# Performance work log

Measured on AMD Instinct MI355X. Metric: run time of the kernel, lower is better.

The kernel has to match this reference:

```python
import jax, jax.numpy as jnp
import numpy as np
from jax import lax

# Key identity used: modulating ALL weights of output channel o by s_o (with no bias
# inside the modulated conv, as in the source where F.conv2d(..., bias=None)) is
# mathematically identical to a plain conv followed by per-(batch, out_channel)
# scaling of the output. This collapses the per-sample Python loop into one conv.

def _upsample2x(x):
    # nearest-neighbor x2, matching F.interpolate(scale_factor=2) default mode
    return jnp.repeat(jnp.repeat(x, 2, axis=2), 2, axis=3)

def _conv(x, w):
    return lax.conv_general_dilated(
        x, w, window_strides=(1, 1), padding=[(1, 1), (1, 1)],
        dimension_numbers=("NCHW", "OIHW", "NCHW"))

def _modconv(x, style, w, fc_w, fc_b):
    # style_fc: [B, style_dim] -> [B, out_ch]
    s = style @ fc_w.T + fc_b          # [B, O]
    y = _conv(x, w)                    # [B, O, H, W]
    return y * s[:, :, None, None]


def setup_inputs() -> dict:
    key = jax.random.key(0)
    ks = jax.random.split(key, 16)
    B, SD = 8, 512
    chans = [(512, 256), (256, 128), (128, 64), (64, 64), (64, 64)]
    inp = {
        "x": jax.random.normal(ks[0], (B, 512, 8, 8), jnp.float32),
        "style": jax.random.normal(ks[1], (B, SD), jnp.float32),
    }
    for i, (ci, co) in enumerate(chans, start=1):
        inp[f"w{i}"] = jax.random.normal(ks[2 * i], (co, ci, 3, 3), jnp.float32) * (1.0 / np.sqrt(ci * 9))
        inp[f"fw{i}"] = jax.random.normal(ks[2 * i + 1], (co, SD), jnp.float32) * (1.0 / np.sqrt(SD))
        inp[f"fb{i}"] = jnp.ones((co,), jnp.float32)
    inp["wf"] = jax.random.normal(ks[12], (3, 64, 3, 3), jnp.float32) * (1.0 / np.sqrt(64 * 9))
    inp["bf"] = jnp.zeros((3,), jnp.float32)
    return inp


def reference(x, style, w1, fw1, fb1, w2, fw2, fb2, w3, fw3, fb3,
              w4, fw4, fb4, w5, fw5, fb5, wf, bf):
    x = _upsample2x(x)
    x = jax.nn.relu(_modconv(x, style, w1, fw1, fb1))
    x = _upsample2x(x)
    x = jax.nn.relu(_modconv(x, style, w2, fw2, fb2))
    x = _upsample2x(x)
    x = jax.nn.relu(_modconv(x, style, w3, fw3, fb3))
    x = _upsample2x(x)
    x = jax.nn.relu(_modconv(x, style, w4, fw4, fb4))
    x = _upsample2x(x)
    x = jax.nn.relu(_modconv(x, style, w5, fw5, fb5))
    x = _conv(x, wf) + bf[None, :, None, None]
    return x
```

## Files before the change

kernel.cpp:

```cpp
#include <hip/hip_runtime.h>
#include <hip/hip_bf16.h>
#include <cstddef>

typedef __bf16 bf16x8 __attribute__((ext_vector_type(8)));
typedef float f32x4 __attribute__((ext_vector_type(4)));

__global__ void prep_all_kernel(const float* __restrict__ x, __hip_bfloat16* __restrict__ act0,
                                const float* __restrict__ w1, __hip_bfloat16* __restrict__ o1,
                                const float* __restrict__ w2, __hip_bfloat16* __restrict__ o2,
                                const float* __restrict__ w3, __hip_bfloat16* __restrict__ o3,
                                const float* __restrict__ w4, __hip_bfloat16* __restrict__ o4,
                                const float* __restrict__ w5, __hip_bfloat16* __restrict__ o5,
                                const float* __restrict__ wf, __hip_bfloat16* __restrict__ of,
                                const float* __restrict__ style,
                                const float* __restrict__ fw1, const float* __restrict__ fb1,
                                const float* __restrict__ fw2, const float* __restrict__ fb2,
                                const float* __restrict__ fw3, const float* __restrict__ fb3,
                                const float* __restrict__ fw4, const float* __restrict__ fb4,
                                const float* __restrict__ fw5, const float* __restrict__ fb5,
                                float* __restrict__ S) {
    const int blk = blockIdx.x;
    if (blk < 1024) {
        int t = blk * 256 + threadIdx.x;
        int c = t & 511; int rest = t >> 9;
        int w = rest & 7; rest >>= 3; int h = rest & 7; int b = rest >> 3;
        act0[t] = __float2bfloat16(x[((b * 512 + c) * 8 + h) * 8 + w]);
    } else if (blk < 12324) {
        int t = (blk - 1024) * 256 + threadIdx.x;
        if (t < 2752512) {
            const float* w; __hip_bfloat16* o; int CI, lgCICH, lgCO16;
            if      (t < 2097152) { w = w1; o = o1; CI = 512; lgCICH = 3; lgCO16 = 4; }
            else if (t < 2621440) { t -= 2097152; w = w2; o = o2; CI = 256; lgCICH = 2; lgCO16 = 3; }
            else                  { t -= 2621440; w = w3; o = o3; CI = 128; lgCICH = 1; lgCO16 = 2; }
            int j    = t & 7;
            int ln   = (t >> 3) & 63;
            int ch   = (t >> 9) & 1;
            int cich = (t >> 10) & ((1 << lgCICH) - 1);
            int co16 = (t >> (10 + lgCICH)) & ((1 << lgCO16) - 1);
            int tap  = (t >> (10 + lgCICH + lgCO16)) & 3;
            int cls  = (t >> (12 + lgCICH + lgCO16)) & 3;
            int co = co16 * 16 + (ln & 15);
            int ci = cich * 64 + ch * 32 + (ln >> 4) * 8 + j;
            int py = cls >> 1, px = cls & 1;
            int i = tap >> 1, jj = tap & 1;
            int r0 = i * (1 + py), rc = py ? (2 - i) : (1 + i);
            int c0 = jj * (1 + px), cc = px ? (2 - jj) : (1 + jj);
            const float* wb = w + ((size_t)co * CI + ci) * 9;
            float s = 0.f;
            for (int rr = 0; rr < rc; ++rr)
                for (int c2 = 0; c2 < cc; ++c2)
                    s += wb[(r0 + rr) * 3 + (c0 + c2)];
            o[t] = __float2bfloat16(s);
        } else if (t < 2883584) {
            int u = t - 2752512;
            const float* w; __hip_bfloat16* o;
            if (u < 65536) { w = w4; o = o4; }
            else           { u -= 65536; w = w5; o = o5; }
            int j   = u & 7;
            int ln  = (u >> 3) & 63;
            int ch  = (u >> 9) & 1;
            int nt  = (u >> 10) & 3;
            int tp  = (u >> 12) & 3;
            int cls = (u >> 14) & 3;
            int py = cls >> 1, px = cls & 1;
            int i = tp >> 1, jj = tp & 1;
            int co = nt * 16 + (ln & 15);
            int ci = ch * 32 + (ln >> 4) * 8 + j;
            int r0 = i * (1 + py), rc = py ? (2 - i) : (1 + i);
            int c0 = jj * (1 + px), cc = px ? (2 - jj) : (1 + jj);
            const float* wb = w + ((size_t)co * 64 + ci) * 9;
            float s = 0.f;
            for (int rr = 0; rr < rc; ++rr)
                for (int c2 = 0; c2 < cc; ++c2)
                    s += wb[(r0 + rr) * 3 + (c0 + c2)];
            o[u] = __float2bfloat16(s);
        } else if (t < 2892800) {
            int u = t - 2883584;
            int j  = u & 7;
            int ln = (u >> 3) & 63;
            int ch = (u >> 9) & 1;
            int tap = u >> 10;
            int rr = ln & 15, qq = ln >> 4;
            int ci = ch * 32 + qq * 8 + j;
            float v = (rr < 3) ? wf[((size_t)rr * 64 + ci) * 9 + tap] : 0.f;
            of[u] = __float2bfloat16(v);
        }
    } else {
        int wvid = (blk - 12324) * 4 + (threadIdx.x >> 6);
        int lane = threadIdx.x & 63;
        const float* fw; const float* fb; int lg, sOff, local;
        if      (wvid < 2048) { fw = fw1; fb = fb1; lg = 8; sOff = 0;    local = wvid; }
        else if (wvid < 3072) { fw = fw2; fb = fb2; lg = 7; sOff = 2048; local = wvid - 2048; }
        else if (wvid < 3584) { fw = fw3; fb = fb3; lg = 6; sOff = 3072; local = wvid - 3072; }
        else if (wvid < 4096) { fw = fw4; fb = fb4; lg = 6; sOff = 3584; local = wvid - 3584; }
        else                  { fw = fw5; fb = fb5; lg = 6; sOff = 4096; local = wvid - 4096; }
        int b = local >> lg, o = local & ((1 << lg) - 1);
        const float* sb = style + b * 512;
        const float* fwo = fw + (size_t)o * 512;
        float p = 0.f;
        #pragma unroll
        for (int k = lane; k < 512; k += 64) p += sb[k] * fwo[k];
        #pragma unroll
        for (int off = 32; off > 0; off >>= 1) p += __shfl_down(p, off);
        if (lane == 0) S[sOff + local] = p + fb[o];
    }
}

template <int CI, int CO, int HS, int WS>
__launch_bounds__(512)
__global__ void conv_partial_kernel(const __hip_bfloat16* __restrict__ actIn,
                                    const __hip_bfloat16* __restrict__ wpk,
                                    float* __restrict__ Part) {
    constexpr int HO = HS * 2, WO = WS * 2;
    constexpr size_t sliceN = (size_t)8 * HO * WO * CO;
    constexpr int CICH = CI / 64, CO16 = CO / 16;

    const int tid = threadIdx.x;
    const int lane = tid & 63, wv = tid >> 6;
    const int r = lane & 15, q = lane >> 4;
    const int rs = r >> 3, sc = r & 7;
    const int lane8 = lane * 8;
    const int cls = wv >> 1, half = wv & 1;
    const int py = cls >> 1, px = cls & 1;

    const int pw = WO / 16, ppb = (HO / 16) * pw;
    const int b = blockIdx.x / ppb;
    const int prest = blockIdx.x - b * ppb;
    const int ph = prest / pw, pwi = prest - ph * pw;
    const int oh0 = ph * 16, ow0 = pwi * 16;
    const int sh0 = oh0 >> 1, sw0 = ow0 >> 1;
    const int n0 = blockIdx.y * 64;
    const int cich = blockIdx.z;
    const int ciOff = cich * 64;

    __shared__ alignas(16) __hip_bfloat16 Tile[100 * 72];

    f32x4 acc[2][4];
    #pragma unroll
    for (int i = 0; i < 2; ++i)
        #pragma unroll
        for (int j = 0; j < 4; ++j) acc[i][j] = f32x4{0.f, 0.f, 0.f, 0.f};

    for (int i = tid; i < 800; i += 512) {
        int pix = i >> 3, koct = i & 7;
        int tr = pix / 10, tc2 = pix - tr * 10;
        int su = sh0 - 1 + tr, sv = sw0 - 1 + tc2;
        uint4 v = {0, 0, 0, 0};
        if (su >= 0 && su < HS && sv >= 0 && sv < WS)
            v = *(const uint4*)(actIn + ((size_t)((b * HS + su) * WS + sv) * CI + ciOff + koct * 8));
        *(uint4*)&Tile[pix * 72 + koct * 8] = v;
    }
    __syncthreads();

    bf16x8 bA[4][2], bB[4][2];

    auto loadB = [&](bf16x8 (&dst)[4][2], int tp) {
        #pragma unroll
        for (int nt = 0; nt < 4; ++nt) {
            const int co16g = (n0 >> 4) + nt;
            #pragma unroll
            for (int ch = 0; ch < 2; ++ch)
                dst[nt][ch] = *(const bf16x8*)(wpk +
                    ((size_t)((((cls * 4 + tp) * CO16 + co16g) * CICH + cich) * 2 + ch) << 9) + lane8);
        }
    };

    auto compute = [&](int tp, bf16x8 (&bfr)[4][2]) {
        const int i = tp >> 1, j = tp & 1;
        const int ro = i + py, co2 = j + px;
        int apix[2];
        #pragma unroll
        for (int mt = 0; mt < 2; ++mt)
            apix[mt] = (2 * (half * 2 + mt) + rs + ro) * 10 + (sc + co2);
        #pragma unroll
        for (int ch = 0; ch < 2; ++ch) {
            bf16x8 af[2];
            #pragma unroll
            for (int mt = 0; mt < 2; ++mt)
                af[mt] = *(const bf16x8*)&Tile[apix[mt] * 72 + ch * 32 + q * 8];
            #pragma unroll
            for (int mt = 0; mt < 2; ++mt)
                #pragma unroll
                for (int nt = 0; nt < 4; ++nt)
                    acc[mt][nt] = __builtin_amdgcn_mfma_f32_16x16x32_bf16(
                        af[mt], bfr[nt][ch], acc[mt][nt], 0, 0, 0);
        }
    };

    loadB(bA, 0);
    loadB(bB, 1);
    compute(0, bA);
    loadB(bA, 2);
    compute(1, bB);
    loadB(bB, 3);
    compute(2, bA);
    compute(3, bB);

    float* P = Part + (size_t)blockIdx.z * sliceN;
    #pragma unroll
    for (int mt = 0; mt < 2; ++mt) {
        #pragma unroll
        for (int t2 = 0; t2 < 4; ++t2) {
            const int m = q * 4 + t2;
            const int row = oh0 + 2 * (2 * (half * 2 + mt) + (m >> 3)) + py;
            const int col = ow0 + 2 * (m & 7) + px;
            const size_t obase = ((size_t)(b * HO + row) * WO + col) * CO + n0;
            #pragma unroll
            for (int nt = 0; nt < 4; ++nt)
                P[obase + nt * 16 + r] = acc[mt][nt][t2];
        }
    }
}

template <int KS, int CO, int HW>
__launch_bounds__(256)
__global__ void reduce_kernel(const float* __restrict__ Part, const float* __restrict__ S,
                              __hip_bfloat16* __restrict__ actOut) {
    constexpr size_t sliceN = (size_t)8 * HW * CO;
    size_t e = ((size_t)blockIdx.x * 256 + threadIdx.x) * 4;
    if (e >= sliceN) return;
    f32x4 sum = {0.f, 0.f, 0.f, 0.f};
    #pragma unroll
    for (int k = 0; k < KS; ++k) sum += *(const f32x4*)(Part + (size_t)k * sliceN + e);
    const int co = (int)(e & (CO - 1));
    const int b = (int)(e / ((size_t)HW * CO));
    const float* Sb = S + b * CO + co;
    union { ushort4 u; __hip_bfloat16 h[4]; } pack;
    #pragma unroll
    for (int j = 0; j < 4; ++j)
        pack.h[j] = __float2bfloat16(fmaxf(sum[j] * Sb[j], 0.f));
    *(ushort4*)((unsigned short*)actOut + e) = pack.u;
}

__launch_bounds__(256)
__global__ void conv_s3_kernel(const __hip_bfloat16* __restrict__ actIn,
                               const __hip_bfloat16* __restrict__ wpk,
                               const float* __restrict__ S,
                               __hip_bfloat16* __restrict__ actOut) {
    constexpr int HS = 32, WS = 32, CI = 128, CO16 = 4, CICH = 2;

    const int tid = threadIdx.x;
    const int lane = tid & 63, wv = tid >> 6;
    const int r = lane & 15, q = lane >> 4;
    const int rr2 = r >> 2, cc2 = r & 3;
    const int lane8 = lane * 8;
    const int py = wv >> 1, px = wv & 1;

    const int b = blockIdx.x >> 6;
    const int prest = blockIdx.x & 63;
    const int ph = prest >> 3, pwi = prest & 7;
    const int oh0 = ph * 8, ow0 = pwi * 8;
    const int sh0 = oh0 >> 1, sw0 = ow0 >> 1;

    __shared__ alignas(16) __hip_bfloat16 Tile[36 * 72];

    f32x4 acc[4];
    #pragma unroll
    for (int j = 0; j < 4; ++j) acc[j] = f32x4{0.f, 0.f, 0.f, 0.f};

    bf16x8 bA[4][2], bB[4][2];

    #pragma unroll 1
    for (int cich = 0; cich < CICH; ++cich) {
        if (cich) __syncthreads();
        for (int i = tid; i < 288; i += 256) {
            int pix = i >> 3, koct = i & 7;
            int tr = pix / 6, tc2 = pix - tr * 6;
            int su = sh0 - 1 + tr, sv = sw0 - 1 + tc2;
            uint4 v = {0, 0, 0, 0};
            if (su >= 0 && su < HS && sv >= 0 && sv < WS)
                v = *(const uint4*)(actIn +
                    ((size_t)((b * HS + su) * WS + sv) * CI + cich * 64 + koct * 8));
            *(uint4*)&Tile[pix * 72 + koct * 8] = v;
        }
        __syncthreads();

        auto loadB = [&](bf16x8 (&dst)[4][2], int tp) {
            #pragma unroll
            for (int nt = 0; nt < 4; ++nt)
                #pragma unroll
                for (int ch = 0; ch < 2; ++ch)
                    dst[nt][ch] = *(const bf16x8*)(wpk +
                        ((size_t)((((wv * 4 + tp) * CO16 + nt) * CICH + cich) * 2 + ch) << 9) + lane8);
        };

        auto compute = [&](int tp, bf16x8 (&bfr)[4][2]) {
            const int i = tp >> 1, j = tp & 1;
            const int apix = (rr2 + i + py) * 6 + (cc2 + j + px);
            #pragma unroll
            for (int ch = 0; ch < 2; ++ch) {
                bf16x8 af = *(const bf16x8*)&Tile[apix * 72 + ch * 32 + q * 8];
                #pragma unroll
                for (int nt = 0; nt < 4; ++nt)
                    acc[nt] = __builtin_amdgcn_mfma_f32_16x16x32_bf16(
                        af, bfr[nt][ch], acc[nt], 0, 0, 0);
            }
        };

        loadB(bA, 0);
        loadB(bB, 1);
        compute(0, bA);
        loadB(bA, 2);
        compute(1, bB);
        loadB(bB, 3);
        compute(2, bA);
        compute(3, bB);
    }

    float sv_[4];
    #pragma unroll
    for (int nt = 0; nt < 4; ++nt) sv_[nt] = S[b * 64 + nt * 16 + r];
    #pragma unroll
    for (int t2 = 0; t2 < 4; ++t2) {
        const int m = q * 4 + t2;
        const int row = oh0 + 2 * (m >> 2) + py;
        const int col = ow0 + 2 * (m & 3) + px;
        const size_t obase = ((size_t)(b * 64 + row) * 64 + col) * 64;
        #pragma unroll
        for (int nt = 0; nt < 4; ++nt)
            actOut[obase + nt * 16 + r] =
                __float2bfloat16(fmaxf(acc[nt][t2] * sv_[nt], 0.f));
    }
}

template <int HS, int WS>
__launch_bounds__(256)
__global__ void conv_patch_kernel(const __hip_bfloat16* __restrict__ actIn,
                                  const __hip_bfloat16* __restrict__ wpk,
                                  const float* __restrict__ S,
                                  __hip_bfloat16* __restrict__ actOut) {
    constexpr int HO = HS * 2, WO = WS * 2;

    const int tid = threadIdx.x;
    const int lane = tid & 63, wv = tid >> 6;
    const int r = lane & 15, q = lane >> 4;
    const int rs = r >> 3, sc = r & 7;
    const int lane8 = lane * 8;
    const int py = wv >> 1, px = wv & 1;

    const int pw = WO / 16, ppb = (HO / 16) * pw;
    const int b = blockIdx.x / ppb;
    const int prest = blockIdx.x - b * ppb;
    const int ph = prest / pw, pwi = prest - ph * pw;
    const int oh0 = ph * 16, ow0 = pwi * 16;
    const int sh0 = oh0 >> 1, sw0 = ow0 >> 1;

    __shared__ alignas(16) __hip_bfloat16 Tile[100 * 72];

    f32x4 acc[4][4];
    #pragma unroll
    for (int i = 0; i < 4; ++i)
        #pragma unroll
        for (int j = 0; j < 4; ++j) acc[i][j] = f32x4{0.f, 0.f, 0.f, 0.f};

    for (int i = tid; i < 800; i += 256) {
        int pix = i >> 3, koct = i & 7;
        int tr = pix / 10, tc2 = pix - tr * 10;
        int su = sh0 - 1 + tr, sv = sw0 - 1 + tc2;
        uint4 v = {0, 0, 0, 0};
        if (su >= 0 && su < HS && sv >= 0 && sv < WS)
            v = *(const uint4*)(actIn + ((size_t)((b * HS + su) * WS + sv) * 64 + koct * 8));
        *(uint4*)&Tile[pix * 72 + koct * 8] = v;
    }
    __syncthreads();

    const __hip_bfloat16* wcls = wpk + ((size_t)wv << 14);

    bf16x8 bA[4][2], bB[4][2];

    auto loadB = [&](bf16x8 (&dst)[4][2], int tp) {
        #pragma unroll
        for (int nt = 0; nt < 4; ++nt)
            #pragma unroll
            for (int ch = 0; ch < 2; ++ch)
                dst[nt][ch] = *(const bf16x8*)(wcls + (tp << 12) + ((nt * 2 + ch) << 9) + lane8);
    };

    auto compute = [&](int tp, bf16x8 (&bfr)[4][2]) {
        const int i = tp >> 1, j = tp & 1;
        const int ro = i + py, co2 = j + px;
        int apix[4];
        #pragma unroll
        for (int mt = 0; mt < 4; ++mt)
            apix[mt] = (2 * mt + rs + ro) * 10 + (sc + co2);
        #pragma unroll
        for (int ch = 0; ch < 2; ++ch) {
            bf16x8 af[4];
            #pragma unroll
            for (int mt = 0; mt < 4; ++mt)
                af[mt] = *(const bf16x8*)&Tile[apix[mt] * 72 + ch * 32 + q * 8];
            #pragma unroll
            for (int mt = 0; mt < 4; ++mt)
                #pragma unroll
                for (int nt = 0; nt < 4; ++nt)
                    acc[mt][nt] = __builtin_amdgcn_mfma_f32_16x16x32_bf16(
                        af[mt], bfr[nt][ch], acc[mt][nt], 0, 0, 0);
        }
    };

    loadB(bA, 0);
    loadB(bB, 1);
    compute(0, bA);
    loadB(bA, 2);
    compute(1, bB);
    loadB(bB, 3);
    compute(2, bA);
    compute(3, bB);

    float sv_[4];
    #pragma unroll
    for (int nt = 0; nt < 4; ++nt) sv_[nt] = S[b * 64 + nt * 16 + r];
    #pragma unroll
    for (int mt = 0; mt < 4; ++mt) {
        #pragma unroll
        for (int t2 = 0; t2 < 4; ++t2) {
            const int m = q * 4 + t2;
            const int row = oh0 + 4 * mt + 2 * (m >> 3) + py;
            const int col = ow0 + 2 * (m & 7) + px;
            const size_t obase = ((size_t)(b * HO + row) * WO + col) * 64;
            #pragma unroll
            for (int nt = 0; nt < 4; ++nt)
                actOut[obase + nt * 16 + r] =
                    __float2bfloat16(fmaxf(acc[mt][nt][t2] * sv_[nt], 0.f));
        }
    }
}

__launch_bounds__(512)
__global__ void conv_s5f_kernel(const __hip_bfloat16* __restrict__ actIn,
                                const __hip_bfloat16* __restrict__ wpk5,
                                const __hip_bfloat16* __restrict__ wpkF,
                                const float* __restrict__ S,
                                const float* __restrict__ bias,
                                float* __restrict__ out) {
    constexpr int HS = 128, WS = 128;

    const int tid = threadIdx.x;
    const int lane = tid & 63, wv = tid >> 6;
    const int r = lane & 15, q = lane >> 4;
    const int lane8 = lane * 8;
    const int cls = wv >> 1, half = wv & 1;
    const int py = cls >> 1, px = cls & 1;

    const int bid = blockIdx.x;
    const int b = bid >> 8;
    const int rest = bid & 255;
    const int oh0 = (rest >> 4) * 16, ow0 = (rest & 15) * 16;
    const int sh0 = oh0 >> 1, sw0 = ow0 >> 1;

    __shared__ alignas(16) __hip_bfloat16 Lds[18 * 18 * 72];
    __hip_bfloat16* TileA = Lds;

    for (int i = tid; i < 800; i += 512) {
        int pix = i >> 3, koct = i & 7;
        int tr = pix / 10, tc2 = pix - tr * 10;
        int su = sh0 - 1 + tr, sv = sw0 - 1 + tc2;
        uint4 v = {0, 0, 0, 0};
        if (su >= 0 && su < HS && sv >= 0 && sv < WS)
            v = *(const uint4*)(actIn + ((size_t)((b * HS + su) * WS + sv) * 64 + koct * 8));
        *(uint4*)&TileA[pix * 72 + koct * 8] = v;
    }
    __syncthreads();

    f32x4 acc[3][4];
    #pragma unroll
    for (int i = 0; i < 3; ++i)
        #pragma unroll
        for (int j = 0; j < 4; ++j) acc[i][j] = f32x4{0.f, 0.f, 0.f, 0.f};

    int jrA[3], jcA[3];
    #pragma unroll
    for (int mt = 0; mt < 3; ++mt) {
        int pm = half * 48 + mt * 16 + r;
        pm = pm > 80 ? 80 : pm;
        jrA[mt] = (pm * 57) >> 9;
        jcA[mt] = pm - jrA[mt] * 9;
    }

    const __hip_bfloat16* wcls = wpk5 + ((size_t)cls << 14);

    bf16x8 bA[4][2], bB[4][2];

    auto loadB = [&](bf16x8 (&dst)[4][2], int tp) {
        #pragma unroll
        for (int nt = 0; nt < 4; ++nt)
            #pragma unroll
            for (int ch = 0; ch < 2; ++ch)
                dst[nt][ch] = *(const bf16x8*)(wcls + (tp << 12) + ((nt * 2 + ch) << 9) + lane8);
    };

    auto compute = [&](int tp, bf16x8 (&bfr)[4][2]) {
        const int i = tp >> 1, j = tp & 1;
        int apix[3];
        #pragma unroll
        for (int mt = 0; mt < 3; ++mt)
            apix[mt] = (jrA[mt] + i) * 10 + (jcA[mt] + j);
        #pragma unroll
        for (int ch = 0; ch < 2; ++ch) {
            bf16x8 af[3];
            #pragma unroll
            for (int mt = 0; mt < 3; ++mt)
                af[mt] = *(const bf16x8*)&TileA[apix[mt] * 72 + ch * 32 + q * 8];
            #pragma unroll
            for (int mt = 0; mt < 3; ++mt)
                #pragma unroll
                for (int nt = 0; nt < 4; ++nt)
                    acc[mt][nt] = __builtin_amdgcn_mfma_f32_16x16x32_bf16(
                        af[mt], bfr[nt][ch], acc[mt][nt], 0, 0, 0);
        }
    };

    loadB(bA, 0);
    loadB(bB, 1);
    compute(0, bA);
    loadB(bA, 2);
    compute(1, bB);
    loadB(bB, 3);
    compute(2, bA);
    compute(3, bB);

    float sv_[4];
    #pragma unroll
    for (int nt = 0; nt < 4; ++nt) sv_[nt] = S[b * 64 + nt * 16 + r];

    __syncthreads();

    #pragma unroll
    for (int mt = 0; mt < 3; ++mt) {
        #pragma unroll
        for (int t2 = 0; t2 < 4; ++t2) {
            const int m = half * 48 + mt * 16 + q * 4 + t2;
            if (m < 81) {
                const int jr = (m * 57) >> 9;
                const int jc = m - jr * 9;
                const int p  = py ? (oh0 - 1 + 2 * jr) : (oh0 + 2 * jr);
                const int pc = px ? (ow0 - 1 + 2 * jc) : (ow0 + 2 * jc);
                const bool valid = (p >= 0) && (p < 256) && (pc >= 0) && (pc < 256);
                const int dpx = (2 * jr + 1 - py) * 18 + (2 * jc + 1 - px);
                #pragma unroll
                for (int nt = 0; nt < 4; ++nt) {
                    float v = valid ? fmaxf(acc[mt][nt][t2] * sv_[nt], 0.f) : 0.f;
                    Lds[dpx * 72 + nt * 16 + r] = __float2bfloat16(v);
                }
            }
        }
    }
    __syncthreads();

    f32x4 acc2[2];
    acc2[0] = f32x4{0.f, 0.f, 0.f, 0.f};
    acc2[1] = f32x4{0.f, 0.f, 0.f, 0.f};

    #pragma unroll 1
    for (int tap = 0; tap < 9; ++tap) {
        const int dyv = tap / 3;
        const int dxv = tap - dyv * 3;
        const int tc = r + dxv;
        int apix[2];
        #pragma unroll
        for (int mt = 0; mt < 2; ++mt)
            apix[mt] = (wv * 2 + mt + dyv) * 18 + tc;
        #pragma unroll
        for (int ch = 0; ch < 2; ++ch) {
            bf16x8 bfr = *(const bf16x8*)(wpkF + ((tap * 2 + ch) << 9) + lane8);
            #pragma unroll
            for (int mt = 0; mt < 2; ++mt) {
                bf16x8 af = *(const bf16x8*)&Lds[apix[mt] * 72 + ch * 32 + q * 8];
                acc2[mt] = __builtin_amdgcn_mfma_f32_16x16x32_bf16(af, bfr, acc2[mt], 0, 0, 0);
            }
        }
    }

    if (r < 3) {
        const float bs = bias[r];
        #pragma unroll
        for (int mt = 0; mt < 2; ++mt) {
            const int prow = oh0 + wv * 2 + mt;
            #pragma unroll
            for (int t2 = 0; t2 < 4; ++t2)
                out[((size_t)(b * 3 + r) << 16) + prow * 256 + ow0 + q * 4 + t2] =
                    acc2[mt][t2] + bs;
        }
    }
}

extern "C" void kernel_launch(void* const* d_in, const int* in_sizes, int n_in,
                              void* d_out, int out_size, void* d_ws, size_t ws_size,
                              hipStream_t stream) {
    const float* x    = (const float*)d_in[0];
    const float* sty  = (const float*)d_in[1];
    const float* w1   = (const float*)d_in[2];
    const float* fw1  = (const float*)d_in[3];
    const float* fb1  = (const float*)d_in[4];
    const float* w2   = (const float*)d_in[5];
    const float* fw2  = (const float*)d_in[6];
    const float* fb2  = (const float*)d_in[7];
    const float* w3   = (const float*)d_in[8];
    const float* fw3  = (const float*)d_in[9];
    const float* fb3  = (const float*)d_in[10];
    const float* w4   = (const float*)d_in[11];
    const float* fw4  = (const float*)d_in[12];
    const float* fb4  = (const float*)d_in[13];
    const float* w5   = (const float*)d_in[14];
    const float* fw5  = (const float*)d_in[15];
    const float* fb5  = (const float*)d_in[16];
    const float* wf   = (const float*)d_in[17];
    const float* bf   = (const float*)d_in[18];
    float* out = (float*)d_out;

    char* ws = (char*)d_ws;
    size_t off = 0;
    auto alloc = [&](size_t bytes) {
        char* p = ws + off;
        off += (bytes + 255) & ~(size_t)255;
        return p;
    };
    float* S1 = (float*)alloc(8 * 256 * 4);
    float* S2 = (float*)alloc(8 * 128 * 4);
    float* S3 = (float*)alloc(8 * 64 * 4);
    float* S4 = (float*)alloc(8 * 64 * 4);
    float* S5 = (float*)alloc(8 * 64 * 4);
    __hip_bfloat16* act0 = (__hip_bfloat16*)alloc((size_t)262144 * 2);
    __hip_bfloat16* act1 = (__hip_bfloat16*)alloc((size_t)524288 * 2);
    __hip_bfloat16* act2 = (__hip_bfloat16*)alloc((size_t)1048576 * 2);
    __hip_bfloat16* act3 = (__hip_bfloat16*)alloc((size_t)2097152 * 2);
    __hip_bfloat16* act4 = (__hip_bfloat16*)alloc((size_t)8388608 * 2);
    __hip_bfloat16* act5 = (__hip_bfloat16*)alloc((size_t)33554432 * 2);
    __hip_bfloat16* wt1  = (__hip_bfloat16*)alloc((size_t)2097152 * 2);
    __hip_bfloat16* wt2  = (__hip_bfloat16*)alloc((size_t)524288 * 2);
    __hip_bfloat16* wt3  = (__hip_bfloat16*)alloc((size_t)131072 * 2);
    __hip_bfloat16* wt4  = (__hip_bfloat16*)alloc((size_t)65536 * 2);
    __hip_bfloat16* wt5  = (__hip_bfloat16*)alloc((size_t)65536 * 2);
    __hip_bfloat16* wtF  = (__hip_bfloat16*)alloc((size_t)9 * 16 * 64 * 2);
    if (off > ws_size) return;

    float* Part = (float*)act5;

    prep_all_kernel<<<13476, 256, 0, stream>>>(x, act0,
                                               w1, wt1, w2, wt2, w3, wt3,
                                               w4, wt4, w5, wt5, wf, wtF,
                                               sty, fw1, fb1, fw2, fb2, fw3, fb3,
                                               fw4, fb4, fw5, fb5, S1);

    conv_partial_kernel<512, 256, 8, 8><<<dim3(8, 4, 8), 512, 0, stream>>>(act0, wt1, Part);
    reduce_kernel<8, 256, 256><<<512, 256, 0, stream>>>(Part, S1, act1);
    conv_partial_kernel<256, 128, 16, 16><<<dim3(32, 2, 4), 512, 0, stream>>>(act1, wt2, Part);
    reduce_kernel<4, 128, 1024><<<1024, 256, 0, stream>>>(Part, S2, act2);

    conv_s3_kernel<<<512, 256, 0, stream>>>(act2, wt3, S3, act3);

    conv_patch_kernel<64, 64><<<dim3(512), 256, 0, stream>>>(act3, wt4, S4, act4);

    conv_s5f_kernel<<<2048, 512, 0, stream>>>(act4, wt5, wtF, S5, bf, out);
}
```

Measured before the change: 197.1 us.

## Replace split-K partial convs plus reduce with fused full-K conv kernels

Layers 1–3 now use one templated conv kernel that loops over all input-channel chunks inside a block, then applies the style scale and ReLU and writes bf16 directly. This drops the fp32 partial-sum buffers and the two separate reduce launches, removing their global-memory round trips and launch overhead. Layers 1 and 2 lose the split-K parallelism and use smaller 8x8 tiles with fewer output channels per block (NT=1 or 2), so each block runs a longer serial K loop and weight reuse per block is lower.

```diff
diff --git a/kernel.cpp b/kernel.cpp
--- a/kernel.cpp
+++ b/kernel.cpp
@@ -106,138 +106,15 @@
     }
 }
 
-template <int CI, int CO, int HS, int WS>
-__launch_bounds__(512)
-__global__ void conv_partial_kernel(const __hip_bfloat16* __restrict__ actIn,
-                                    const __hip_bfloat16* __restrict__ wpk,
-                                    float* __restrict__ Part) {
-    constexpr int HO = HS * 2, WO = WS * 2;
-    constexpr size_t sliceN = (size_t)8 * HO * WO * CO;
+template <int HS, int CI, int CO, int NT>
+__launch_bounds__(256)
+__global__ void conv_sfull_kernel(const __hip_bfloat16* __restrict__ actIn,
+                                  const __hip_bfloat16* __restrict__ wpk,
+                                  const float* __restrict__ S,
+                                  __hip_bfloat16* __restrict__ actOut) {
+    constexpr int WS = HS, HO = HS * 2;
     constexpr int CICH = CI / 64, CO16 = CO / 16;
-
-    const int tid = threadIdx.x;
-    const int lane = tid & 63, wv = tid >> 6;
-    const int r = lane & 15, q = lane >> 4;
-    const int rs = r >> 3, sc = r & 7;
-    const int lane8 = lane * 8;
-    const int cls = wv >> 1, half = wv & 1;
-    const int py = cls >> 1, px = cls & 1;
-
-    const int pw = WO / 16, ppb = (HO / 16) * pw;
-    const int b = blockIdx.x / ppb;
-    const int prest = blockIdx.x - b * ppb;
-    const int ph = prest / pw, pwi = prest - ph * pw;
-    const int oh0 = ph * 16, ow0 = pwi * 16;
-    const int sh0 = oh0 >> 1, sw0 = ow0 >> 1;
-    const int n0 = blockIdx.y * 64;
-    const int cich = blockIdx.z;
-    const int ciOff = cich * 64;
-
-    __shared__ alignas(16) __hip_bfloat16 Tile[100 * 72];
-
-    f32x4 acc[2][4];
-    #pragma unroll
-    for (int i = 0; i < 2; ++i)
-        #pragma unroll
-        for (int j = 0; j < 4; ++j) acc[i][j] = f32x4{0.f, 0.f, 0.f, 0.f};
-
-    for (int i = tid; i < 800; i += 512) {
-        int pix = i >> 3, koct = i & 7;
-        int tr = pix / 10, tc2 = pix - tr * 10;
-        int su = sh0 - 1 + tr, sv = sw0 - 1 + tc2;
-        uint4 v = {0, 0, 0, 0};
-        if (su >= 0 && su < HS && sv >= 0 && sv < WS)
-            v = *(const uint4*)(actIn + ((size_t)((b * HS + su) * WS + sv) * CI + ciOff + koct * 8));
-        *(uint4*)&Tile[pix * 72 + koct * 8] = v;
-    }
-    __syncthreads();
-
-    bf16x8 bA[4][2], bB[4][2];
-
-    auto loadB = [&](bf16x8 (&dst)[4][2], int tp) {
-        #pragma unroll
-        for (int nt = 0; nt < 4; ++nt) {
-            const int co16g = (n0 >> 4) + nt;
-            #pragma unroll
-            for (int ch = 0; ch < 2; ++ch)
-                dst[nt][ch] = *(const bf16x8*)(wpk +
-                    ((size_t)((((cls * 4 + tp) * CO16 + co16g) * CICH + cich) * 2 + ch) << 9) + lane8);
-        }
-    };
-
-    auto compute = [&](int tp, bf16x8 (&bfr)[4][2]) {
-        const int i = tp >> 1, j = tp & 1;
-        const int ro = i + py, co2 = j + px;
-        int apix[2];
-        #pragma unroll
-        for (int mt = 0; mt < 2; ++mt)
-            apix[mt] = (2 * (half * 2 + mt) + rs + ro) * 10 + (sc + co2);
-        #pragma unroll
-        for (int ch = 0; ch < 2; ++ch) {
-            bf16x8 af[2];
-            #pragma unroll
-            for (int mt = 0; mt < 2; ++mt)
-                af[mt] = *(const bf16x8*)&Tile[apix[mt] * 72 + ch * 32 + q * 8];
-            #pragma unroll
-            for (int mt = 0; mt < 2; ++mt)
-                #pragma unroll
-                for (int nt = 0; nt < 4; ++nt)
-                    acc[mt][nt] = __builtin_amdgcn_mfma_f32_16x16x32_bf16(
-                        af[mt], bfr[nt][ch], acc[mt][nt], 0, 0, 0);
-        }
-    };
-
-    loadB(bA, 0);
-    loadB(bB, 1);
-    compute(0, bA);
-    loadB(bA, 2);
-    compute(1, bB);
-    loadB(bB, 3);
-    compute(2, bA);
-    compute(3, bB);
-
-    float* P = Part + (size_t)blockIdx.z * sliceN;
-    #pragma unroll
-    for (int mt = 0; mt < 2; ++mt) {
-        #pragma unroll
-        for (int t2 = 0; t2 < 4; ++t2) {
-            const int m = q * 4 + t2;
-            const int row = oh0 + 2 * (2 * (half * 2 + mt) + (m >> 3)) + py;
-            const int col = ow0 + 2 * (m & 7) + px;
-            const size_t obase = ((size_t)(b * HO + row) * WO + col) * CO + n0;
-            #pragma unroll
-            for (int nt = 0; nt < 4; ++nt)
-                P[obase + nt * 16 + r] = acc[mt][nt][t2];
-        }
-    }
-}
-
-template <int KS, int CO, int HW>
-__launch_bounds__(256)
-__global__ void reduce_kernel(const float* __restrict__ Part, const float* __restrict__ S,
-                              __hip_bfloat16* __restrict__ actOut) {
-    constexpr size_t sliceN = (size_t)8 * HW * CO;
-    size_t e = ((size_t)blockIdx.x * 256 + threadIdx.x) * 4;
-    if (e >= sliceN) return;
-    f32x4 sum = {0.f, 0.f, 0.f, 0.f};
-    #pragma unroll
-    for (int k = 0; k < KS; ++k) sum += *(const f32x4*)(Part + (size_t)k * sliceN + e);
-    const int co = (int)(e & (CO - 1));
-    const int b = (int)(e / ((size_t)HW * CO));
-    const float* Sb = S + b * CO + co;
-    union { ushort4 u; __hip_bfloat16 h[4]; } pack;
-    #pragma unroll
-    for (int j = 0; j < 4; ++j)
-        pack.h[j] = __float2bfloat16(fmaxf(sum[j] * Sb[j], 0.f));
-    *(ushort4*)((unsigned short*)actOut + e) = pack.u;
-}
-
-__launch_bounds__(256)
-__global__ void conv_s3_kernel(const __hip_bfloat16* __restrict__ actIn,
-                               const __hip_bfloat16* __restrict__ wpk,
-                               const float* __restrict__ S,
-                               __hip_bfloat16* __restrict__ actOut) {
-    constexpr int HS = 32, WS = 32, CI = 128, CO16 = 4, CICH = 2;
+    constexpr int PW = HO / 8, PPI = PW * PW;
 
     const int tid = threadIdx.x;
     const int lane = tid & 63, wv = tid >> 6;
@@ -246,19 +123,21 @@
     const int lane8 = lane * 8;
     const int py = wv >> 1, px = wv & 1;
 
-    const int b = blockIdx.x >> 6;
-    const int prest = blockIdx.x & 63;
-    const int ph = prest >> 3, pwi = prest & 7;
+    const int b = blockIdx.x / PPI;
+    const int prest = blockIdx.x - b * PPI;
+    const int ph = prest / PW, pwi = prest - ph * PW;
     const int oh0 = ph * 8, ow0 = pwi * 8;
     const int sh0 = oh0 >> 1, sw0 = ow0 >> 1;
+    const int co16base = blockIdx.y * NT;
+    const int n0 = co16base * 16;
 
     __shared__ alignas(16) __hip_bfloat16 Tile[36 * 72];
 
-    f32x4 acc[4];
-    #pragma unroll
-    for (int j = 0; j < 4; ++j) acc[j] = f32x4{0.f, 0.f, 0.f, 0.f};
-
-    bf16x8 bA[4][2], bB[4][2];
+    f32x4 acc[NT];
+    #pragma unroll
+    for (int j = 0; j < NT; ++j) acc[j] = f32x4{0.f, 0.f, 0.f, 0.f};
+
+    bf16x8 bA[NT][2], bB[NT][2];
 
     #pragma unroll 1
     for (int cich = 0; cich < CICH; ++cich) {
@@ -275,23 +154,23 @@
         }
         __syncthreads();
 
-        auto loadB = [&](bf16x8 (&dst)[4][2], int tp) {
-            #pragma unroll
-            for (int nt = 0; nt < 4; ++nt)
+        auto loadB = [&](bf16x8 (&dst)[NT][2], int tp) {
+            #pragma unroll
+            for (int nt = 0; nt < NT; ++nt)
                 #pragma unroll
                 for (int ch = 0; ch < 2; ++ch)
                     dst[nt][ch] = *(const bf16x8*)(wpk +
-                        ((size_t)((((wv * 4 + tp) * CO16 + nt) * CICH + cich) * 2 + ch) << 9) + lane8);
+                        ((size_t)((((wv * 4 + tp) * CO16 + co16base + nt) * CICH + cich) * 2 + ch) << 9) + lane8);
         };
 
-        auto compute = [&](int tp, bf16x8 (&bfr)[4][2]) {
+        auto compute = [&](int tp, bf16x8 (&bfr)[NT][2]) {
             const int i = tp >> 1, j = tp & 1;
             const int apix = (rr2 + i + py) * 6 + (cc2 + j + px);
             #pragma unroll
             for (int ch = 0; ch < 2; ++ch) {
                 bf16x8 af = *(const bf16x8*)&Tile[apix * 72 + ch * 32 + q * 8];
                 #pragma unroll
-                for (int nt = 0; nt < 4; ++nt)
+                for (int nt = 0; nt < NT; ++nt)
                     acc[nt] = __builtin_amdgcn_mfma_f32_16x16x32_bf16(
                         af, bfr[nt][ch], acc[nt], 0, 0, 0);
             }
@@ -307,17 +186,17 @@
         compute(3, bB);
     }
 
-    float sv_[4];
-    #pragma unroll
-    for (int nt = 0; nt < 4; ++nt) sv_[nt] = S[b * 64 + nt * 16 + r];
+    float sv_[NT];
+    #pragma unroll
+    for (int nt = 0; nt < NT; ++nt) sv_[nt] = S[b * CO + n0 + nt * 16 + r];
     #pragma unroll
     for (int t2 = 0; t2 < 4; ++t2) {
         const int m = q * 4 + t2;
         const int row = oh0 + 2 * (m >> 2) + py;
         const int col = ow0 + 2 * (m & 3) + px;
-        const size_t obase = ((size_t)(b * 64 + row) * 64 + col) * 64;
-        #pragma unroll
-        for (int nt = 0; nt < 4; ++nt)
+        const size_t obase = ((size_t)(b * HO + row) * HO + col) * CO + n0;
+        #pragma unroll
+        for (int nt = 0; nt < NT; ++nt)
             actOut[obase + nt * 16 + r] =
                 __float2bfloat16(fmaxf(acc[nt][t2] * sv_[nt], 0.f));
     }
@@ -633,8 +512,7 @@
     __hip_bfloat16* wt5  = (__hip_bfloat16*)alloc((size_t)65536 * 2);
     __hip_bfloat16* wtF  = (__hip_bfloat16*)alloc((size_t)9 * 16 * 64 * 2);
     if (off > ws_size) return;
-
-    float* Part = (float*)act5;
+    (void)act5;
 
     prep_all_kernel<<<13476, 256, 0, stream>>>(x, act0,
                                                w1, wt1, w2, wt2, w3, wt3,
@@ -642,12 +520,9 @@
                                                sty, fw1, fb1, fw2, fb2, fw3, fb3,
                                                fw4, fb4, fw5, fb5, S1);
 
-    conv_partial_kernel<512, 256, 8, 8><<<dim3(8, 4, 8), 512, 0, stream>>>(act0, wt1, Part);
-    reduce_kernel<8, 256, 256><<<512, 256, 0, stream>>>(Part, S1, act1);
-    conv_partial_kernel<256, 128, 16, 16><<<dim3(32, 2, 4), 512, 0, stream>>>(act1, wt2, Part);
-    reduce_kernel<4, 128, 1024><<<1024, 256, 0, stream>>>(Part, S2, act2);
-
-    conv_s3_kernel<<<512, 256, 0, stream>>>(act2, wt3, S3, act3);
+    conv_sfull_kernel<8, 512, 256, 1><<<dim3(32, 16), 256, 0, stream>>>(act0, wt1, S1, act1);
+    conv_sfull_kernel<16, 256, 128, 2><<<dim3(128, 4), 256, 0, stream>>>(act1, wt2, S2, act2);
+    conv_sfull_kernel<32, 128, 64, 4><<<dim3(512, 1), 256, 0, stream>>>(act2, wt3, S3, act3);
 
     conv_patch_kernel<64, 64><<<dim3(512), 256, 0, stream>>>(act3, wt4, S4, act4);
 
```

After: 193.5 us. About the same (-1.8%).
